# Kernel tuning notes

Measured on AMD Instinct MI355X. Metric: run time of the kernel, lower is better.

The kernel has to match this reference:

```python
import jax, jax.numpy as jnp
import numpy as np

NUM_USER = 100000
NUM_ITEM = 50000
EMBED_DIM = 64
NUM_LAYER = 3
NUM_INTERACTIONS = 1600000  # symmetrized -> nnz = 3.2M
BATCH = 4096


def setup_inputs() -> dict:
    key = jax.random.key(0)
    k1, k2, k3, k4, k5, k6 = jax.random.split(key, 6)
    N = NUM_USER + NUM_ITEM
    user_emb = jax.random.normal(k1, (NUM_USER, EMBED_DIM), dtype=jnp.float32) / EMBED_DIM
    item_emb = jax.random.normal(k2, (NUM_ITEM, EMBED_DIM), dtype=jnp.float32) / EMBED_DIM
    # random bipartite interactions, symmetrized adjacency
    u = jax.random.randint(k3, (NUM_INTERACTIONS,), 0, NUM_USER, dtype=jnp.int32)
    i = jax.random.randint(k4, (NUM_INTERACTIONS,), 0, NUM_ITEM, dtype=jnp.int32) + NUM_USER
    adj_rows = jnp.concatenate([u, i])  # [nnz]
    adj_cols = jnp.concatenate([i, u])  # [nnz]
    # symmetric normalization D^-1/2 A D^-1/2
    deg = jax.ops.segment_sum(jnp.ones_like(adj_rows, dtype=jnp.float32), adj_rows, num_segments=N)
    deg = jnp.maximum(deg, 1.0)
    inv_sqrt = 1.0 / jnp.sqrt(deg)
    adj_vals = inv_sqrt[adj_rows] * inv_sqrt[adj_cols]
    user_ids = jax.random.randint(k5, (BATCH,), 0, NUM_USER, dtype=jnp.int32)
    item_ids = jax.random.randint(k6, (BATCH,), 0, NUM_ITEM, dtype=jnp.int32)
    return {"user_emb": user_emb, "item_emb": item_emb, "adj_vals": adj_vals,
            "adj_rows": adj_rows, "adj_cols": adj_cols,
            "user_ids": user_ids, "item_ids": item_ids}


def reference(user_emb, item_emb, adj_vals, adj_rows, adj_cols, user_ids, item_ids):
    num_user = user_emb.shape[0]
    N = num_user + item_emb.shape[0]
    x = jnp.concatenate([user_emb, item_emb], axis=0)  # [N, D]
    acc = x  # running sum == stack+mean over layers, fused
    for _ in range(NUM_LAYER):
        # SpMM: out[r] += vals * x[c]
        x = jax.ops.segment_sum(adj_vals[:, None] * x[adj_cols], adj_rows, num_segments=N)
        acc = acc + x
    emb = acc / (NUM_LAYER + 1)
    batch_user = emb[user_ids]                  # [B, D]
    batch_item = emb[num_user + item_ids]       # [B, D]
    scores = jnp.sum(batch_user * batch_item, axis=-1)  # DotProdScorer
    return scores
```

## Files before the change

kernel.cpp:

```cpp
#include <hip/hip_runtime.h>


#define DIM 64
#define TSHIFT 8
#define TMASK ((1 << TSHIFT) - 1)
#define TPAD 768
#define EWG 6272
#define STAGE_CAP 6272
#define NREP 4
#define RSTR 2560
#define TSTRIDE 10240
#define NI4 7

typedef unsigned short u16;
typedef unsigned char u8;
typedef unsigned int u32;
typedef unsigned int uv4 __attribute__((ext_vector_type(4)));
typedef float f2 __attribute__((ext_vector_type(2)));

__device__ __forceinline__ u32 f2bf(float f) {
  u32 u = __float_as_uint(f);
  return (u + 0x7FFFu + ((u >> 16) & 1u)) >> 16;
}
__device__ __forceinline__ float bflo(u32 u) {
  return __uint_as_float(u << 16);
}
__device__ __forceinline__ float bfhi(u32 u) {
  return __uint_as_float(u & 0xFFFF0000u);
}
__device__ __forceinline__ f2 up2(u32 u) {
  f2 r;
  r.x = bflo(u);
  r.y = bfhi(u);
  return r;
}

__device__ __forceinline__ int block_incl_scan(int lsum, int tid, int* wsum) {
  int lane = tid & 63, wv = tid >> 6;
  int v = lsum;
#pragma unroll
  for (int off = 1; off < 64; off <<= 1) {
    int t = __shfl_up(v, off, 64);
    if (lane >= off) v += t;
  }
  __syncthreads();
  if (lane == 63) wsum[wv] = v;
  __syncthreads();
  int add = 0;
  if (wv > 0) add += wsum[0];
  if (wv > 1) add += wsum[1];
  if (wv > 2) add += wsum[2];
  return v + add;
}


__global__ __launch_bounds__(256) void partition_direct(
    const int* __restrict__ rows, const int* __restrict__ cols, int nnz,
    int T, int* __restrict__ tcur, u32* __restrict__ bucket) {
  __shared__ u32 sorted[STAGE_CAP];
  __shared__ u16 sortedt[STAGE_CAP];
  __shared__ int cnt[TPAD], lstart[TPAD], gbase[TPAD];
  __shared__ int wsum[4];
  int w = blockIdx.x, tid = threadIdx.x;
  int rep = w & (NREP - 1);
  int j0 = tid * 3;
  cnt[j0] = 0; cnt[j0 + 1] = 0; cnt[j0 + 2] = 0;
  __syncthreads();
  int base = w * EWG;
  int end = min(base + EWG, nnz);
  int total = end - base;
  if (total <= 0) return;
  int nv = total >> 2;
  const int4* r4 = (const int4*)(rows + base);
  const int4* c4 = (const int4*)(cols + base);
  int4 rr[NI4];
#pragma unroll
  for (int j = 0; j < NI4; ++j) {
    int i = tid + j * 256;
    if (i < nv) {
      int4 r = r4[i];
      rr[j] = r;
      atomicAdd(&cnt[r.x >> TSHIFT], 1);
      atomicAdd(&cnt[r.y >> TSHIFT], 1);
      atomicAdd(&cnt[r.z >> TSHIFT], 1);
      atomicAdd(&cnt[r.w >> TSHIFT], 1);
    }
  }
  for (int e = base + (nv << 2) + tid; e < end; e += 256)
    atomicAdd(&cnt[rows[e] >> TSHIFT], 1);
  __syncthreads();
  int c0 = cnt[j0], c1 = cnt[j0 + 1], c2 = cnt[j0 + 2];
  int lsum = c0 + c1 + c2;
  int incl = block_incl_scan(lsum, tid, wsum);
  int excl = incl - lsum;
  lstart[j0] = excl;
  lstart[j0 + 1] = excl + c0;
  lstart[j0 + 2] = excl + c0 + c1;
  if (c0 > 0)
    gbase[j0] = j0 * TSTRIDE + rep * RSTR + atomicAdd(&tcur[j0 * NREP + rep], c0);
  if (c1 > 0)
    gbase[j0 + 1] = (j0 + 1) * TSTRIDE + rep * RSTR +
                    atomicAdd(&tcur[(j0 + 1) * NREP + rep], c1);
  if (c2 > 0)
    gbase[j0 + 2] = (j0 + 2) * TSTRIDE + rep * RSTR +
                    atomicAdd(&tcur[(j0 + 2) * NREP + rep], c2);
  cnt[j0] = 0; cnt[j0 + 1] = 0; cnt[j0 + 2] = 0;
  __syncthreads();
#pragma unroll
  for (int j = 0; j < NI4; ++j) {
    int i = tid + j * 256;
    if (i < nv) {
      int4 r = rr[j];
      int4 c = c4[i];
      int t, s, d;
      t = r.x >> TSHIFT; s = atomicAdd(&cnt[t], 1); d = lstart[t] + s;
      sorted[d] = ((u32)(r.x & TMASK) << 18) | (u32)c.x; sortedt[d] = (u16)t;
      t = r.y >> TSHIFT; s = atomicAdd(&cnt[t], 1); d = lstart[t] + s;
      sorted[d] = ((u32)(r.y & TMASK) << 18) | (u32)c.y; sortedt[d] = (u16)t;
      t = r.z >> TSHIFT; s = atomicAdd(&cnt[t], 1); d = lstart[t] + s;
      sorted[d] = ((u32)(r.z & TMASK) << 18) | (u32)c.z; sortedt[d] = (u16)t;
      t = r.w >> TSHIFT; s = atomicAdd(&cnt[t], 1); d = lstart[t] + s;
      sorted[d] = ((u32)(r.w & TMASK) << 18) | (u32)c.w; sortedt[d] = (u16)t;
    }
  }
  for (int e = base + (nv << 2) + tid; e < end; e += 256) {
    int r = rows[e];
    int c = cols[e];
    int t = r >> TSHIFT;
    int s = atomicAdd(&cnt[t], 1);
    int d = lstart[t] + s;
    sorted[d] = ((u32)(r & TMASK) << 18) | (u32)c;
    sortedt[d] = (u16)t;
  }
  __syncthreads();
  for (int i = tid; i < total; i += 256) {
    int t = sortedt[i];
    bucket[(size_t)gbase[t] + (i - lstart[t])] = sorted[i];
  }
}


__global__ __launch_bounds__(256) void build_csr_y0(
    const u32* __restrict__ bucket, const int* __restrict__ tcur, int T,
    int U, int N, const float4* __restrict__ ue, const float4* __restrict__ ie,
    int* __restrict__ row_ptr, u32* __restrict__ csr,
    uint4* __restrict__ y0b) {
  __shared__ int tl[TPAD];
  __shared__ int hist[256];
  __shared__ int cur[256];
  __shared__ int wsum[4];
  int b = blockIdx.x;
  int t = (b & 1) ? (T - 1 - (b >> 1)) : (b >> 1);
  int tid = threadIdx.x;
  int j0 = tid * 3;
  int v0 = 0, v1 = 0, v2 = 0;
  if (j0 < T) {
    int4 q = ((const int4*)tcur)[j0];
    v0 = q.x + q.y + q.z + q.w;
  }
  if (j0 + 1 < T) {
    int4 q = ((const int4*)tcur)[j0 + 1];
    v1 = q.x + q.y + q.z + q.w;
  }
  if (j0 + 2 < T) {
    int4 q = ((const int4*)tcur)[j0 + 2];
    v2 = q.x + q.y + q.z + q.w;
  }
  int lsum = v0 + v1 + v2;
  int incl0 = block_incl_scan(lsum, tid, wsum);
  int excl0 = incl0 - lsum;
  tl[j0] = excl0 + v0;
  tl[j0 + 1] = excl0 + v0 + v1;
  tl[j0 + 2] = excl0 + v0 + v1 + v2;
  hist[tid] = 0;
  __syncthreads();
  int tbase = (t == 0) ? 0 : tl[t - 1];
  int4 rl = ((const int4*)tcur)[t];
#pragma unroll
  for (int rep = 0; rep < NREP; ++rep) {
    int len = (rep == 0) ? rl.x : (rep == 1) ? rl.y : (rep == 2) ? rl.z : rl.w;
    int rs = t * TSTRIDE + rep * RSTR;
    const uint4* b4 = (const uint4*)(bucket + rs);
    int nv = len >> 2;
    for (int i = tid; i < nv; i += 256) {
      uint4 e = b4[i];
      atomicAdd(&hist[e.x >> 18], 1);
      atomicAdd(&hist[e.y >> 18], 1);
      atomicAdd(&hist[e.z >> 18], 1);
      atomicAdd(&hist[e.w >> 18], 1);
    }
    for (int i = rs + (nv << 2) + tid; i < rs + len; i += 256)
      atomicAdd(&hist[bucket[i] >> 18], 1);
  }
  __syncthreads();
  int h = hist[tid];
  int incl = block_incl_scan(h, tid, wsum);
  int r = (t << TSHIFT) + tid;
  if (r < N) row_ptr[r + 1] = tbase + incl;
  if (t == 0 && tid == 0) row_ptr[0] = 0;
  if (b == 0 && tid < 8)
    y0b[(size_t)N * 8 + tid] = make_uint4(0, 0, 0, 0);
  cur[tid] = tbase + incl - h;
  __syncthreads();
  for (int pass = 0; pass < 8; ++pass) {
    int lr = pass * 32 + (tid >> 3);
    int q = tid & 7;
    int row = (t << TSHIFT) + lr;
    if (row < N) {
      float invs = rsqrtf((float)max(hist[lr], 1));
      const float4* src = (row < U) ? (ue + (size_t)row * 16 + q * 2)
                                    : (ie + (size_t)(row - U) * 16 + q * 2);
      float4 a = src[0], bb = src[1];
      uint4 o;
      o.x = f2bf(a.x * invs) | (f2bf(a.y * invs) << 16);
      o.y = f2bf(a.z * invs) | (f2bf(a.w * invs) << 16);
      o.z = f2bf(bb.x * invs) | (f2bf(bb.y * invs) << 16);
      o.w = f2bf(bb.z * invs) | (f2bf(bb.w * invs) << 16);
      y0b[(size_t)row * 8 + q] = o;
    }
  }
#pragma unroll
  for (int rep = 0; rep < NREP; ++rep) {
    int len = (rep == 0) ? rl.x : (rep == 1) ? rl.y : (rep == 2) ? rl.z : rl.w;
    int rs = t * TSTRIDE + rep * RSTR;
    const uint4* b4 = (const uint4*)(bucket + rs);
    int nv = len >> 2;
    for (int i = tid; i < nv; i += 256) {
      uint4 e = b4[i];
      csr[atomicAdd(&cur[e.x >> 18], 1)] = e.x & 0x3FFFFu;
      csr[atomicAdd(&cur[e.y >> 18], 1)] = e.y & 0x3FFFFu;
      csr[atomicAdd(&cur[e.z >> 18], 1)] = e.z & 0x3FFFFu;
      csr[atomicAdd(&cur[e.w >> 18], 1)] = e.w & 0x3FFFFu;
    }
    for (int i = rs + (nv << 2) + tid; i < rs + len; i += 256) {
      u32 e = bucket[i];
      csr[atomicAdd(&cur[e >> 18], 1)] = e & 0x3FFFFu;
    }
  }
}


__device__ __forceinline__ void load_stage(
    u32 (&c)[8], uv4 (&g)[8], int k, int d, int s,
    const u32* __restrict__ csr, const char* __restrict__ yb, u32 soff,
    int n) {
#pragma unroll
  for (int j = 0; j < 8; ++j) c[j] = (k + j < d) ? csr[s + k + j] : (u32)n;
#pragma unroll
  for (int j = 0; j < 8; ++j)
    g[j] = *(const uv4*)(yb + (size_t)(((size_t)c[j] << 7) | soff));
}

#define ACC_STAGE(G)                                                         \
  _Pragma("unroll") for (int j = 0; j < 8; ++j) {                            \
    a0 += up2(G[j].x);                                                       \
    a1 += up2(G[j].y);                                                       \
    a2 += up2(G[j].z);                                                       \
    a3 += up2(G[j].w);                                                       \
  }

__global__ __launch_bounds__(256, 4) void spmm_sum(
    const int* __restrict__ row_ptr, const u32* __restrict__ csr,
    const u16* __restrict__ yin, u16* __restrict__ yout, int n) {
  if (blockIdx.x == 0 && threadIdx.x < 8)
    ((uint4*)(yout + (size_t)n * DIM))[threadIdx.x] = make_uint4(0, 0, 0, 0);
  int row = (blockIdx.x * 256 + threadIdx.x) >> 3;
  int q8 = threadIdx.x & 7;
  if (row >= n) return;
  int s = row_ptr[row];
  int d = row_ptr[row + 1] - s;
  const char* yb = (const char*)yin;
  u32 soff = (u32)q8 << 4;
  f2 a0 = 0.f, a1 = 0.f, a2 = 0.f, a3 = 0.f;
  u32 cA[8], cB[8];
  uv4 gA[8], gB[8];
  if (d > 0) {
    load_stage(cA, gA, 0, d, s, csr, yb, soff, n);
    int k = 8;
    while (k < d) {
      load_stage(cB, gB, k, d, s, csr, yb, soff, n);
      k += 8;
      ACC_STAGE(gA)
      if (k >= d) {
        ACC_STAGE(gB)
        goto done;
      }
      load_stage(cA, gA, k, d, s, csr, yb, soff, n);
      k += 8;
      ACC_STAGE(gB)
    }
    ACC_STAGE(gA)
  }
done:;
  float inv = 1.0f / (float)max(d, 1);
  uint4 o;
  o.x = f2bf(a0.x * inv) | (f2bf(a0.y * inv) << 16);
  o.y = f2bf(a1.x * inv) | (f2bf(a1.y * inv) << 16);
  o.z = f2bf(a2.x * inv) | (f2bf(a2.y * inv) << 16);
  o.w = f2bf(a3.x * inv) | (f2bf(a3.y * inv) << 16);
  ((uint4*)(yout + (size_t)row * DIM))[q8] = o;
}


#define ACC8(G)                                                              \
  s0 += bflo(G.x); s1 += bfhi(G.x);                                          \
  s2 += bflo(G.y); s3 += bfhi(G.y);                                          \
  s4 += bflo(G.z); s5 += bfhi(G.z);                                          \
  s6 += bflo(G.w); s7 += bfhi(G.w);

__device__ __forceinline__ void gather8(
    const int* __restrict__ row_ptr, const u32* __restrict__ csr,
    const u16* __restrict__ y, int row, int s, int q8, int n, float* o) {
  int start = row_ptr[row];
  int end = row_ptr[row + 1];
  float s0 = 0.f, s1 = 0.f, s2 = 0.f, s3 = 0.f;
  float s4 = 0.f, s5 = 0.f, s6 = 0.f, s7 = 0.f;
  for (int k = start + s; k < end; k += 16) {
    int k2 = k + 8;
    bool ok2 = k2 < end;
    u32 c0 = csr[k];
    u32 c1 = ok2 ? csr[k2] : (u32)n;
    uint4 g0 = ((const uint4*)(y + (size_t)c0 * DIM))[q8];
    uint4 g1 = ((const uint4*)(y + (size_t)c1 * DIM))[q8];
    ACC8(g0) ACC8(g1)
  }
  for (int m = 8; m <= 32; m <<= 1) {
    s0 += __shfl_xor(s0, m, 64); s1 += __shfl_xor(s1, m, 64);
    s2 += __shfl_xor(s2, m, 64); s3 += __shfl_xor(s3, m, 64);
    s4 += __shfl_xor(s4, m, 64); s5 += __shfl_xor(s5, m, 64);
    s6 += __shfl_xor(s6, m, 64); s7 += __shfl_xor(s7, m, 64);
  }
  o[0] = s0; o[1] = s1; o[2] = s2; o[3] = s3;
  o[4] = s4; o[5] = s5; o[6] = s6; o[7] = s7;
}

__global__ __launch_bounds__(256) void spmm3_score(
    const int* __restrict__ row_ptr, const u32* __restrict__ csr,
    const float* __restrict__ ue, const float* __restrict__ ie,
    const u16* __restrict__ y1b, const u16* __restrict__ y2b,
    const int* __restrict__ user_ids, const int* __restrict__ item_ids,
    int U, int N, int batch, float* __restrict__ out) {
  __shared__ float ab[2][2][64];
  int tid = threadIdx.x;
  int pl = tid >> 7;
  int side = (tid >> 6) & 1;
  int lane = tid & 63;
  int w = blockIdx.x * 2 + pl;
  bool active = w < batch;
  int s = lane >> 3;
  int q8 = lane & 7;
  if (active) {
    int u = user_ids[w];
    int iti = item_ids[w];
    int row = (side == 0) ? u : iti + U;
    float g[8];
    gather8(row_ptr, csr, y2b, row, s, q8, N, g);
    int dd = row_ptr[row + 1] - row_ptr[row];
    float sd = sqrtf((float)max(dd, 1)), rd = 1.0f / sd;
    const float4* pe = (side == 0)
                           ? (const float4*)(ue + (size_t)u * DIM) + q8 * 2
                           : (const float4*)(ie + (size_t)iti * DIM) + q8 * 2;
    float4 ea = pe[0], eb = pe[1];
    uint4 y1v = ((const uint4*)(y1b + (size_t)row * DIM))[q8];
    uint4 y2v = ((const uint4*)(y2b + (size_t)row * DIM))[q8];
    if (s == 0) {
      float* dst = &ab[pl][side][q8 * 8];
      dst[0] = ea.x + sd * (bflo(y1v.x) + bflo(y2v.x)) + rd * g[0];
      dst[1] = ea.y + sd * (bfhi(y1v.x) + bfhi(y2v.x)) + rd * g[1];
      dst[2] = ea.z + sd * (bflo(y1v.y) + bflo(y2v.y)) + rd * g[2];
      dst[3] = ea.w + sd * (bfhi(y1v.y) + bfhi(y2v.y)) + rd * g[3];
      dst[4] = eb.x + sd * (bflo(y1v.z) + bflo(y2v.z)) + rd * g[4];
      dst[5] = eb.y + sd * (bfhi(y1v.z) + bfhi(y2v.z)) + rd * g[5];
      dst[6] = eb.z + sd * (bflo(y1v.w) + bflo(y2v.w)) + rd * g[6];
      dst[7] = eb.w + sd * (bfhi(y1v.w) + bfhi(y2v.w)) + rd * g[7];
    }
  }
  __syncthreads();
  if (active && side == 0) {
    float p = ab[pl][0][lane] * ab[pl][1][lane];
    p += __shfl_xor(p, 1, 64);
    p += __shfl_xor(p, 2, 64);
    p += __shfl_xor(p, 4, 64);
    p += __shfl_xor(p, 8, 64);
    p += __shfl_xor(p, 16, 64);
    p += __shfl_xor(p, 32, 64);
    if (lane == 0) out[w] = p * (1.0f / 16.0f);
  }
}

extern "C" void kernel_launch(void* const* d_in, const int* in_sizes, int n_in,
                              void* d_out, int out_size, void* d_ws, size_t ws_size,
                              hipStream_t stream) {
  const float* user_emb = (const float*)d_in[0];
  const float* item_emb = (const float*)d_in[1];
  const int* adj_rows = (const int*)d_in[3];
  const int* adj_cols = (const int*)d_in[4];
  const int* user_ids = (const int*)d_in[5];
  const int* item_ids = (const int*)d_in[6];
  float* scores = (float*)d_out;

  const int U = in_sizes[0] / DIM;
  const int I = in_sizes[1] / DIM;
  const int N = U + I;
  const int nnz = in_sizes[2];
  const int B = in_sizes[5];

  const int T = (N + TMASK) >> TSHIFT;
  const int npw = (nnz + EWG - 1) / EWG;

  char* p = (char*)d_ws;
  auto carve = [&](size_t bytes) {
    void* r = (void*)p;
    p += (bytes + 255) & ~(size_t)255;
    return r;
  };
  u16* y0b = (u16*)carve((size_t)(N + 1) * DIM * 2);
  u16* y1b = (u16*)carve((size_t)(N + 1) * DIM * 2);
  u16* y2b = (u16*)carve((size_t)(N + 1) * DIM * 2);
  int* row_ptr = (int*)carve((size_t)(N + 1) * 4);
  int* tcur = (int*)carve((size_t)T * NREP * 4);
  u32* bucket = (u32*)carve((size_t)(T + 1) * TSTRIDE * 4);
  u32* csr = (u32*)carve((size_t)nnz * 4);

  hipMemsetAsync(tcur, 0, (size_t)T * NREP * 4, stream);

  partition_direct<<<npw, 256, 0, stream>>>(adj_rows, adj_cols, nnz, T, tcur,
                                            bucket);

  build_csr_y0<<<T, 256, 0, stream>>>(bucket, tcur, T, U, N,
                                      (const float4*)user_emb,
                                      (const float4*)item_emb, row_ptr,
                                      csr, (uint4*)y0b);

  const int sblocks = (N * 8 + 255) / 256;
  spmm_sum<<<sblocks, 256, 0, stream>>>(row_ptr, csr, y0b, y1b, N);
  spmm_sum<<<sblocks, 256, 0, stream>>>(row_ptr, csr, y1b, y2b, N);

  spmm3_score<<<(B + 1) / 2, 256, 0, stream>>>(row_ptr, csr, user_emb,
                                               item_emb, y1b, y2b, user_ids,
                                               item_ids, U, N, B, scores);
}
```

Baseline: 265.9 us.

## Fuse all stages into one persistent kernel with software grid barriers

Replaces the five separate kernel launches (partition, CSR build, two SpMM passes, scoring) with a single persistent kernel of fixed grid size that runs each stage in turn, separated by atomic-counter grid barriers. A shared-memory union lets each phase reuse the same LDS. The aim is to remove launch gaps and per-kernel tail drain. In exchange it depends on all 768 blocks being co-resident to avoid deadlock, the larger LDS footprint may lower occupancy in the SpMM phases, and those phases now loop over virtual blocks.

```diff
diff --git a/kernel.cpp b/kernel.cpp
--- a/kernel.cpp
+++ b/kernel.cpp
@@ -11,6 +11,7 @@
 #define RSTR 2560
 #define TSTRIDE 10240
 #define NI4 7
+#define GRID 768
 
 typedef unsigned short u16;
 typedef unsigned char u8;
@@ -33,6 +34,34 @@
   r.x = bflo(u);
   r.y = bfhi(u);
   return r;
+}
+
+union SM {
+  struct {
+    u32 sorted[STAGE_CAP];
+    u16 sortedt[STAGE_CAP];
+    int cnt[TPAD], lstart[TPAD], gbase[TPAD], wsum[4];
+  } part;
+  struct {
+    int tl[TPAD], hist[256], cur[256], wsum[4];
+  } bld;
+  struct {
+    float ab[2][2][64];
+  } sc;
+};
+
+__device__ __forceinline__ void grid_barrier(int* g_arrive, int target) {
+  __syncthreads();
+  if (threadIdx.x == 0) {
+    __threadfence();
+    __hip_atomic_fetch_add(g_arrive, 1, __ATOMIC_ACQ_REL,
+                           __HIP_MEMORY_SCOPE_AGENT);
+    while (__hip_atomic_load(g_arrive, __ATOMIC_ACQUIRE,
+                             __HIP_MEMORY_SCOPE_AGENT) < target)
+      __builtin_amdgcn_s_sleep(8);
+    __threadfence();
+  }
+  __syncthreads();
 }
 
 __device__ __forceinline__ int block_incl_scan(int lsum, int tid, int* wsum) {
@@ -54,192 +83,6 @@
 }
 
 
-__global__ __launch_bounds__(256) void partition_direct(
-    const int* __restrict__ rows, const int* __restrict__ cols, int nnz,
-    int T, int* __restrict__ tcur, u32* __restrict__ bucket) {
-  __shared__ u32 sorted[STAGE_CAP];
-  __shared__ u16 sortedt[STAGE_CAP];
-  __shared__ int cnt[TPAD], lstart[TPAD], gbase[TPAD];
-  __shared__ int wsum[4];
-  int w = blockIdx.x, tid = threadIdx.x;
-  int rep = w & (NREP - 1);
-  int j0 = tid * 3;
-  cnt[j0] = 0; cnt[j0 + 1] = 0; cnt[j0 + 2] = 0;
-  __syncthreads();
-  int base = w * EWG;
-  int end = min(base + EWG, nnz);
-  int total = end - base;
-  if (total <= 0) return;
-  int nv = total >> 2;
-  const int4* r4 = (const int4*)(rows + base);
-  const int4* c4 = (const int4*)(cols + base);
-  int4 rr[NI4];
-#pragma unroll
-  for (int j = 0; j < NI4; ++j) {
-    int i = tid + j * 256;
-    if (i < nv) {
-      int4 r = r4[i];
-      rr[j] = r;
-      atomicAdd(&cnt[r.x >> TSHIFT], 1);
-      atomicAdd(&cnt[r.y >> TSHIFT], 1);
-      atomicAdd(&cnt[r.z >> TSHIFT], 1);
-      atomicAdd(&cnt[r.w >> TSHIFT], 1);
-    }
-  }
-  for (int e = base + (nv << 2) + tid; e < end; e += 256)
-    atomicAdd(&cnt[rows[e] >> TSHIFT], 1);
-  __syncthreads();
-  int c0 = cnt[j0], c1 = cnt[j0 + 1], c2 = cnt[j0 + 2];
-  int lsum = c0 + c1 + c2;
-  int incl = block_incl_scan(lsum, tid, wsum);
-  int excl = incl - lsum;
-  lstart[j0] = excl;
-  lstart[j0 + 1] = excl + c0;
-  lstart[j0 + 2] = excl + c0 + c1;
-  if (c0 > 0)
-    gbase[j0] = j0 * TSTRIDE + rep * RSTR + atomicAdd(&tcur[j0 * NREP + rep], c0);
-  if (c1 > 0)
-    gbase[j0 + 1] = (j0 + 1) * TSTRIDE + rep * RSTR +
-                    atomicAdd(&tcur[(j0 + 1) * NREP + rep], c1);
-  if (c2 > 0)
-    gbase[j0 + 2] = (j0 + 2) * TSTRIDE + rep * RSTR +
-                    atomicAdd(&tcur[(j0 + 2) * NREP + rep], c2);
-  cnt[j0] = 0; cnt[j0 + 1] = 0; cnt[j0 + 2] = 0;
-  __syncthreads();
-#pragma unroll
-  for (int j = 0; j < NI4; ++j) {
-    int i = tid + j * 256;
-    if (i < nv) {
-      int4 r = rr[j];
-      int4 c = c4[i];
-      int t, s, d;
-      t = r.x >> TSHIFT; s = atomicAdd(&cnt[t], 1); d = lstart[t] + s;
-      sorted[d] = ((u32)(r.x & TMASK) << 18) | (u32)c.x; sortedt[d] = (u16)t;
-      t = r.y >> TSHIFT; s = atomicAdd(&cnt[t], 1); d = lstart[t] + s;
-      sorted[d] = ((u32)(r.y & TMASK) << 18) | (u32)c.y; sortedt[d] = (u16)t;
-      t = r.z >> TSHIFT; s = atomicAdd(&cnt[t], 1); d = lstart[t] + s;
-      sorted[d] = ((u32)(r.z & TMASK) << 18) | (u32)c.z; sortedt[d] = (u16)t;
-      t = r.w >> TSHIFT; s = atomicAdd(&cnt[t], 1); d = lstart[t] + s;
-      sorted[d] = ((u32)(r.w & TMASK) << 18) | (u32)c.w; sortedt[d] = (u16)t;
-    }
-  }
-  for (int e = base + (nv << 2) + tid; e < end; e += 256) {
-    int r = rows[e];
-    int c = cols[e];
-    int t = r >> TSHIFT;
-    int s = atomicAdd(&cnt[t], 1);
-    int d = lstart[t] + s;
-    sorted[d] = ((u32)(r & TMASK) << 18) | (u32)c;
-    sortedt[d] = (u16)t;
-  }
-  __syncthreads();
-  for (int i = tid; i < total; i += 256) {
-    int t = sortedt[i];
-    bucket[(size_t)gbase[t] + (i - lstart[t])] = sorted[i];
-  }
-}
-
-
-__global__ __launch_bounds__(256) void build_csr_y0(
-    const u32* __restrict__ bucket, const int* __restrict__ tcur, int T,
-    int U, int N, const float4* __restrict__ ue, const float4* __restrict__ ie,
-    int* __restrict__ row_ptr, u32* __restrict__ csr,
-    uint4* __restrict__ y0b) {
-  __shared__ int tl[TPAD];
-  __shared__ int hist[256];
-  __shared__ int cur[256];
-  __shared__ int wsum[4];
-  int b = blockIdx.x;
-  int t = (b & 1) ? (T - 1 - (b >> 1)) : (b >> 1);
-  int tid = threadIdx.x;
-  int j0 = tid * 3;
-  int v0 = 0, v1 = 0, v2 = 0;
-  if (j0 < T) {
-    int4 q = ((const int4*)tcur)[j0];
-    v0 = q.x + q.y + q.z + q.w;
-  }
-  if (j0 + 1 < T) {
-    int4 q = ((const int4*)tcur)[j0 + 1];
-    v1 = q.x + q.y + q.z + q.w;
-  }
-  if (j0 + 2 < T) {
-    int4 q = ((const int4*)tcur)[j0 + 2];
-    v2 = q.x + q.y + q.z + q.w;
-  }
-  int lsum = v0 + v1 + v2;
-  int incl0 = block_incl_scan(lsum, tid, wsum);
-  int excl0 = incl0 - lsum;
-  tl[j0] = excl0 + v0;
-  tl[j0 + 1] = excl0 + v0 + v1;
-  tl[j0 + 2] = excl0 + v0 + v1 + v2;
-  hist[tid] = 0;
-  __syncthreads();
-  int tbase = (t == 0) ? 0 : tl[t - 1];
-  int4 rl = ((const int4*)tcur)[t];
-#pragma unroll
-  for (int rep = 0; rep < NREP; ++rep) {
-    int len = (rep == 0) ? rl.x : (rep == 1) ? rl.y : (rep == 2) ? rl.z : rl.w;
-    int rs = t * TSTRIDE + rep * RSTR;
-    const uint4* b4 = (const uint4*)(bucket + rs);
-    int nv = len >> 2;
-    for (int i = tid; i < nv; i += 256) {
-      uint4 e = b4[i];
-      atomicAdd(&hist[e.x >> 18], 1);
-      atomicAdd(&hist[e.y >> 18], 1);
-      atomicAdd(&hist[e.z >> 18], 1);
-      atomicAdd(&hist[e.w >> 18], 1);
-    }
-    for (int i = rs + (nv << 2) + tid; i < rs + len; i += 256)
-      atomicAdd(&hist[bucket[i] >> 18], 1);
-  }
-  __syncthreads();
-  int h = hist[tid];
-  int incl = block_incl_scan(h, tid, wsum);
-  int r = (t << TSHIFT) + tid;
-  if (r < N) row_ptr[r + 1] = tbase + incl;
-  if (t == 0 && tid == 0) row_ptr[0] = 0;
-  if (b == 0 && tid < 8)
-    y0b[(size_t)N * 8 + tid] = make_uint4(0, 0, 0, 0);
-  cur[tid] = tbase + incl - h;
-  __syncthreads();
-  for (int pass = 0; pass < 8; ++pass) {
-    int lr = pass * 32 + (tid >> 3);
-    int q = tid & 7;
-    int row = (t << TSHIFT) + lr;
-    if (row < N) {
-      float invs = rsqrtf((float)max(hist[lr], 1));
-      const float4* src = (row < U) ? (ue + (size_t)row * 16 + q * 2)
-                                    : (ie + (size_t)(row - U) * 16 + q * 2);
-      float4 a = src[0], bb = src[1];
-      uint4 o;
-      o.x = f2bf(a.x * invs) | (f2bf(a.y * invs) << 16);
-      o.y = f2bf(a.z * invs) | (f2bf(a.w * invs) << 16);
-      o.z = f2bf(bb.x * invs) | (f2bf(bb.y * invs) << 16);
-      o.w = f2bf(bb.z * invs) | (f2bf(bb.w * invs) << 16);
-      y0b[(size_t)row * 8 + q] = o;
-    }
-  }
-#pragma unroll
-  for (int rep = 0; rep < NREP; ++rep) {
-    int len = (rep == 0) ? rl.x : (rep == 1) ? rl.y : (rep == 2) ? rl.z : rl.w;
-    int rs = t * TSTRIDE + rep * RSTR;
-    const uint4* b4 = (const uint4*)(bucket + rs);
-    int nv = len >> 2;
-    for (int i = tid; i < nv; i += 256) {
-      uint4 e = b4[i];
-      csr[atomicAdd(&cur[e.x >> 18], 1)] = e.x & 0x3FFFFu;
-      csr[atomicAdd(&cur[e.y >> 18], 1)] = e.y & 0x3FFFFu;
-      csr[atomicAdd(&cur[e.z >> 18], 1)] = e.z & 0x3FFFFu;
-      csr[atomicAdd(&cur[e.w >> 18], 1)] = e.w & 0x3FFFFu;
-    }
-    for (int i = rs + (nv << 2) + tid; i < rs + len; i += 256) {
-      u32 e = bucket[i];
-      csr[atomicAdd(&cur[e >> 18], 1)] = e & 0x3FFFFu;
-    }
-  }
-}
-
-
 __device__ __forceinline__ void load_stage(
     u32 (&c)[8], uv4 (&g)[8], int k, int d, int s,
     const u32* __restrict__ csr, const char* __restrict__ yb, u32 soff,
@@ -259,46 +102,49 @@
     a3 += up2(G[j].w);                                                       \
   }
 
-__global__ __launch_bounds__(256, 4) void spmm_sum(
-    const int* __restrict__ row_ptr, const u32* __restrict__ csr,
-    const u16* __restrict__ yin, u16* __restrict__ yout, int n) {
+__device__ void spmm_phase(const int* __restrict__ row_ptr,
+                           const u32* __restrict__ csr,
+                           const u16* __restrict__ yin,
+                           u16* __restrict__ yout, int n, int sblocks) {
   if (blockIdx.x == 0 && threadIdx.x < 8)
     ((uint4*)(yout + (size_t)n * DIM))[threadIdx.x] = make_uint4(0, 0, 0, 0);
-  int row = (blockIdx.x * 256 + threadIdx.x) >> 3;
-  int q8 = threadIdx.x & 7;
-  if (row >= n) return;
-  int s = row_ptr[row];
-  int d = row_ptr[row + 1] - s;
-  const char* yb = (const char*)yin;
-  u32 soff = (u32)q8 << 4;
-  f2 a0 = 0.f, a1 = 0.f, a2 = 0.f, a3 = 0.f;
-  u32 cA[8], cB[8];
-  uv4 gA[8], gB[8];
-  if (d > 0) {
-    load_stage(cA, gA, 0, d, s, csr, yb, soff, n);
-    int k = 8;
-    while (k < d) {
-      load_stage(cB, gB, k, d, s, csr, yb, soff, n);
-      k += 8;
+  for (int vb = blockIdx.x; vb < sblocks; vb += GRID) {
+    int row = (vb * 256 + threadIdx.x) >> 3;
+    int q8 = threadIdx.x & 7;
+    if (row >= n) continue;
+    int s = row_ptr[row];
+    int d = row_ptr[row + 1] - s;
+    const char* yb = (const char*)yin;
+    u32 soff = (u32)q8 << 4;
+    f2 a0 = 0.f, a1 = 0.f, a2 = 0.f, a3 = 0.f;
+    u32 cA[8], cB[8];
+    uv4 gA[8], gB[8];
+    if (d > 0) {
+      load_stage(cA, gA, 0, d, s, csr, yb, soff, n);
+      int k = 8;
+      while (k < d) {
+        load_stage(cB, gB, k, d, s, csr, yb, soff, n);
+        k += 8;
+        ACC_STAGE(gA)
+        if (k >= d) {
+          ACC_STAGE(gB)
+          goto done;
+        }
+        load_stage(cA, gA, k, d, s, csr, yb, soff, n);
+        k += 8;
+        ACC_STAGE(gB)
+      }
       ACC_STAGE(gA)
-      if (k >= d) {
-        ACC_STAGE(gB)
-        goto done;
-      }
-      load_stage(cA, gA, k, d, s, csr, yb, soff, n);
-      k += 8;
-      ACC_STAGE(gB)
     }
-    ACC_STAGE(gA)
-  }
-done:;
-  float inv = 1.0f / (float)max(d, 1);
-  uint4 o;
-  o.x = f2bf(a0.x * inv) | (f2bf(a0.y * inv) << 16);
-  o.y = f2bf(a1.x * inv) | (f2bf(a1.y * inv) << 16);
-  o.z = f2bf(a2.x * inv) | (f2bf(a2.y * inv) << 16);
-  o.w = f2bf(a3.x * inv) | (f2bf(a3.y * inv) << 16);
-  ((uint4*)(yout + (size_t)row * DIM))[q8] = o;
+  done:;
+    float inv = 1.0f / (float)max(d, 1);
+    uint4 o;
+    o.x = f2bf(a0.x * inv) | (f2bf(a0.y * inv) << 16);
+    o.y = f2bf(a1.x * inv) | (f2bf(a1.y * inv) << 16);
+    o.z = f2bf(a2.x * inv) | (f2bf(a2.y * inv) << 16);
+    o.w = f2bf(a3.x * inv) | (f2bf(a3.y * inv) << 16);
+    ((uint4*)(yout + (size_t)row * DIM))[q8] = o;
+  }
 }
 
 
@@ -334,79 +180,279 @@
   o[4] = s4; o[5] = s5; o[6] = s6; o[7] = s7;
 }
 
-__global__ __launch_bounds__(256) void spmm3_score(
-    const int* __restrict__ row_ptr, const u32* __restrict__ csr,
-    const float* __restrict__ ue, const float* __restrict__ ie,
-    const u16* __restrict__ y1b, const u16* __restrict__ y2b,
-    const int* __restrict__ user_ids, const int* __restrict__ item_ids,
-    int U, int N, int batch, float* __restrict__ out) {
-  __shared__ float ab[2][2][64];
+
+__global__ __launch_bounds__(256, 3) void lightgcn_fused(
+    const int* __restrict__ rows, const int* __restrict__ cols, int nnz,
+    int T, int npw, const float4* __restrict__ ue,
+    const float4* __restrict__ ie, const int* __restrict__ user_ids,
+    const int* __restrict__ item_ids, int U, int N, int B,
+    int* __restrict__ tcur, int* g_arrive, u32* __restrict__ bucket,
+    int* __restrict__ row_ptr, u32* __restrict__ csr, u16* __restrict__ y0b,
+    u16* __restrict__ y1b, u16* __restrict__ y2b, float* __restrict__ out) {
+  __shared__ SM sm;
   int tid = threadIdx.x;
-  int pl = tid >> 7;
-  int side = (tid >> 6) & 1;
-  int lane = tid & 63;
-  int w = blockIdx.x * 2 + pl;
-  bool active = w < batch;
-  int s = lane >> 3;
-  int q8 = lane & 7;
-  if (active) {
-    int u = user_ids[w];
-    int iti = item_ids[w];
-    int row = (side == 0) ? u : iti + U;
-    float g[8];
-    gather8(row_ptr, csr, y2b, row, s, q8, N, g);
-    int dd = row_ptr[row + 1] - row_ptr[row];
-    float sd = sqrtf((float)max(dd, 1)), rd = 1.0f / sd;
-    const float4* pe = (side == 0)
-                           ? (const float4*)(ue + (size_t)u * DIM) + q8 * 2
-                           : (const float4*)(ie + (size_t)iti * DIM) + q8 * 2;
-    float4 ea = pe[0], eb = pe[1];
-    uint4 y1v = ((const uint4*)(y1b + (size_t)row * DIM))[q8];
-    uint4 y2v = ((const uint4*)(y2b + (size_t)row * DIM))[q8];
-    if (s == 0) {
-      float* dst = &ab[pl][side][q8 * 8];
-      dst[0] = ea.x + sd * (bflo(y1v.x) + bflo(y2v.x)) + rd * g[0];
-      dst[1] = ea.y + sd * (bfhi(y1v.x) + bfhi(y2v.x)) + rd * g[1];
-      dst[2] = ea.z + sd * (bflo(y1v.y) + bflo(y2v.y)) + rd * g[2];
-      dst[3] = ea.w + sd * (bfhi(y1v.y) + bfhi(y2v.y)) + rd * g[3];
-      dst[4] = eb.x + sd * (bflo(y1v.z) + bflo(y2v.z)) + rd * g[4];
-      dst[5] = eb.y + sd * (bfhi(y1v.z) + bfhi(y2v.z)) + rd * g[5];
-      dst[6] = eb.z + sd * (bflo(y1v.w) + bflo(y2v.w)) + rd * g[6];
-      dst[7] = eb.w + sd * (bfhi(y1v.w) + bfhi(y2v.w)) + rd * g[7];
+
+  {
+    int w = blockIdx.x;
+    if (w < npw) {
+      int rep = w & (NREP - 1);
+      int j0 = tid * 3;
+      sm.part.cnt[j0] = 0; sm.part.cnt[j0 + 1] = 0; sm.part.cnt[j0 + 2] = 0;
+      __syncthreads();
+      int base = w * EWG;
+      int end = min(base + EWG, nnz);
+      int total = end - base;
+      int nv = total >> 2;
+      const int4* r4 = (const int4*)(rows + base);
+      const int4* c4 = (const int4*)(cols + base);
+      int4 rr[NI4];
+#pragma unroll
+      for (int j = 0; j < NI4; ++j) {
+        int i = tid + j * 256;
+        if (i < nv) {
+          int4 r = r4[i];
+          rr[j] = r;
+          atomicAdd(&sm.part.cnt[r.x >> TSHIFT], 1);
+          atomicAdd(&sm.part.cnt[r.y >> TSHIFT], 1);
+          atomicAdd(&sm.part.cnt[r.z >> TSHIFT], 1);
+          atomicAdd(&sm.part.cnt[r.w >> TSHIFT], 1);
+        }
+      }
+      for (int e = base + (nv << 2) + tid; e < end; e += 256)
+        atomicAdd(&sm.part.cnt[rows[e] >> TSHIFT], 1);
+      __syncthreads();
+      int c0 = sm.part.cnt[j0], c1 = sm.part.cnt[j0 + 1],
+          c2 = sm.part.cnt[j0 + 2];
+      int lsum = c0 + c1 + c2;
+      int incl = block_incl_scan(lsum, tid, sm.part.wsum);
+      int excl = incl - lsum;
+      sm.part.lstart[j0] = excl;
+      sm.part.lstart[j0 + 1] = excl + c0;
+      sm.part.lstart[j0 + 2] = excl + c0 + c1;
+      if (c0 > 0)
+        sm.part.gbase[j0] = j0 * TSTRIDE + rep * RSTR +
+                            atomicAdd(&tcur[j0 * NREP + rep], c0);
+      if (c1 > 0)
+        sm.part.gbase[j0 + 1] = (j0 + 1) * TSTRIDE + rep * RSTR +
+                                atomicAdd(&tcur[(j0 + 1) * NREP + rep], c1);
+      if (c2 > 0)
+        sm.part.gbase[j0 + 2] = (j0 + 2) * TSTRIDE + rep * RSTR +
+                                atomicAdd(&tcur[(j0 + 2) * NREP + rep], c2);
+      sm.part.cnt[j0] = 0; sm.part.cnt[j0 + 1] = 0; sm.part.cnt[j0 + 2] = 0;
+      __syncthreads();
+#pragma unroll
+      for (int j = 0; j < NI4; ++j) {
+        int i = tid + j * 256;
+        if (i < nv) {
+          int4 r = rr[j];
+          int4 c = c4[i];
+          int t, s, d;
+          t = r.x >> TSHIFT; s = atomicAdd(&sm.part.cnt[t], 1);
+          d = sm.part.lstart[t] + s;
+          sm.part.sorted[d] = ((u32)(r.x & TMASK) << 18) | (u32)c.x;
+          sm.part.sortedt[d] = (u16)t;
+          t = r.y >> TSHIFT; s = atomicAdd(&sm.part.cnt[t], 1);
+          d = sm.part.lstart[t] + s;
+          sm.part.sorted[d] = ((u32)(r.y & TMASK) << 18) | (u32)c.y;
+          sm.part.sortedt[d] = (u16)t;
+          t = r.z >> TSHIFT; s = atomicAdd(&sm.part.cnt[t], 1);
+          d = sm.part.lstart[t] + s;
+          sm.part.sorted[d] = ((u32)(r.z & TMASK) << 18) | (u32)c.z;
+          sm.part.sortedt[d] = (u16)t;
+          t = r.w >> TSHIFT; s = atomicAdd(&sm.part.cnt[t], 1);
+          d = sm.part.lstart[t] + s;
+          sm.part.sorted[d] = ((u32)(r.w & TMASK) << 18) | (u32)c.w;
+          sm.part.sortedt[d] = (u16)t;
+        }
+      }
+      for (int e = base + (nv << 2) + tid; e < end; e += 256) {
+        int r = rows[e];
+        int c = cols[e];
+        int t = r >> TSHIFT;
+        int s = atomicAdd(&sm.part.cnt[t], 1);
+        int d = sm.part.lstart[t] + s;
+        sm.part.sorted[d] = ((u32)(r & TMASK) << 18) | (u32)c;
+        sm.part.sortedt[d] = (u16)t;
+      }
+      __syncthreads();
+      for (int i = tid; i < total; i += 256) {
+        int t = sm.part.sortedt[i];
+        bucket[(size_t)sm.part.gbase[t] + (i - sm.part.lstart[t])] =
+            sm.part.sorted[i];
+      }
     }
   }
-  __syncthreads();
-  if (active && side == 0) {
-    float p = ab[pl][0][lane] * ab[pl][1][lane];
-    p += __shfl_xor(p, 1, 64);
-    p += __shfl_xor(p, 2, 64);
-    p += __shfl_xor(p, 4, 64);
-    p += __shfl_xor(p, 8, 64);
-    p += __shfl_xor(p, 16, 64);
-    p += __shfl_xor(p, 32, 64);
-    if (lane == 0) out[w] = p * (1.0f / 16.0f);
+  grid_barrier(g_arrive, GRID);
+
+  {
+    int b = blockIdx.x;
+    if (b < T) {
+      int t = (b & 1) ? (T - 1 - (b >> 1)) : (b >> 1);
+      int j0 = tid * 3;
+      int v0 = 0, v1 = 0, v2 = 0;
+      if (j0 < T) {
+        int4 q = ((const int4*)tcur)[j0];
+        v0 = q.x + q.y + q.z + q.w;
+      }
+      if (j0 + 1 < T) {
+        int4 q = ((const int4*)tcur)[j0 + 1];
+        v1 = q.x + q.y + q.z + q.w;
+      }
+      if (j0 + 2 < T) {
+        int4 q = ((const int4*)tcur)[j0 + 2];
+        v2 = q.x + q.y + q.z + q.w;
+      }
+      int lsum = v0 + v1 + v2;
+      int incl0 = block_incl_scan(lsum, tid, sm.bld.wsum);
+      int excl0 = incl0 - lsum;
+      sm.bld.tl[j0] = excl0 + v0;
+      sm.bld.tl[j0 + 1] = excl0 + v0 + v1;
+      sm.bld.tl[j0 + 2] = excl0 + v0 + v1 + v2;
+      sm.bld.hist[tid] = 0;
+      __syncthreads();
+      int tbase = (t == 0) ? 0 : sm.bld.tl[t - 1];
+      int4 rl = ((const int4*)tcur)[t];
+#pragma unroll
+      for (int rep = 0; rep < NREP; ++rep) {
+        int len =
+            (rep == 0) ? rl.x : (rep == 1) ? rl.y : (rep == 2) ? rl.z : rl.w;
+        int rs = t * TSTRIDE + rep * RSTR;
+        const uint4* b4 = (const uint4*)(bucket + rs);
+        int nv = len >> 2;
+        for (int i = tid; i < nv; i += 256) {
+          uint4 e = b4[i];
+          atomicAdd(&sm.bld.hist[e.x >> 18], 1);
+          atomicAdd(&sm.bld.hist[e.y >> 18], 1);
+          atomicAdd(&sm.bld.hist[e.z >> 18], 1);
+          atomicAdd(&sm.bld.hist[e.w >> 18], 1);
+        }
+        for (int i = rs + (nv << 2) + tid; i < rs + len; i += 256)
+          atomicAdd(&sm.bld.hist[bucket[i] >> 18], 1);
+      }
+      __syncthreads();
+      int h = sm.bld.hist[tid];
+      int incl = block_incl_scan(h, tid, sm.bld.wsum);
+      int r = (t << TSHIFT) + tid;
+      if (r < N) row_ptr[r + 1] = tbase + incl;
+      if (t == 0 && tid == 0) row_ptr[0] = 0;
+      if (b == 0 && tid < 8)
+        ((uint4*)y0b)[(size_t)N * 8 + tid] = make_uint4(0, 0, 0, 0);
+      sm.bld.cur[tid] = tbase + incl - h;
+      __syncthreads();
+      for (int pass = 0; pass < 8; ++pass) {
+        int lr = pass * 32 + (tid >> 3);
+        int q = tid & 7;
+        int row = (t << TSHIFT) + lr;
+        if (row < N) {
+          float invs = rsqrtf((float)max(sm.bld.hist[lr], 1));
+          const float4* src = (row < U)
+                                  ? (ue + (size_t)row * 16 + q * 2)
+                                  : (ie + (size_t)(row - U) * 16 + q * 2);
+          float4 a = src[0], bb = src[1];
+          uint4 o;
+          o.x = f2bf(a.x * invs) | (f2bf(a.y * invs) << 16);
+          o.y = f2bf(a.z * invs) | (f2bf(a.w * invs) << 16);
+          o.z = f2bf(bb.x * invs) | (f2bf(bb.y * invs) << 16);
+          o.w = f2bf(bb.z * invs) | (f2bf(bb.w * invs) << 16);
+          ((uint4*)y0b)[(size_t)row * 8 + q] = o;
+        }
+      }
+#pragma unroll
+      for (int rep = 0; rep < NREP; ++rep) {
+        int len =
+            (rep == 0) ? rl.x : (rep == 1) ? rl.y : (rep == 2) ? rl.z : rl.w;
+        int rs = t * TSTRIDE + rep * RSTR;
+        const uint4* b4 = (const uint4*)(bucket + rs);
+        int nv = len >> 2;
+        for (int i = tid; i < nv; i += 256) {
+          uint4 e = b4[i];
+          csr[atomicAdd(&sm.bld.cur[e.x >> 18], 1)] = e.x & 0x3FFFFu;
+          csr[atomicAdd(&sm.bld.cur[e.y >> 18], 1)] = e.y & 0x3FFFFu;
+          csr[atomicAdd(&sm.bld.cur[e.z >> 18], 1)] = e.z & 0x3FFFFu;
+          csr[atomicAdd(&sm.bld.cur[e.w >> 18], 1)] = e.w & 0x3FFFFu;
+        }
+        for (int i = rs + (nv << 2) + tid; i < rs + len; i += 256) {
+          u32 e = bucket[i];
+          csr[atomicAdd(&sm.bld.cur[e >> 18], 1)] = e & 0x3FFFFu;
+        }
+      }
+    }
+  }
+  grid_barrier(g_arrive, 2 * GRID);
+
+  const int sblocks = (N * 8 + 255) / 256;
+  spmm_phase(row_ptr, csr, y0b, y1b, N, sblocks);
+  grid_barrier(g_arrive, 3 * GRID);
+  spmm_phase(row_ptr, csr, y1b, y2b, N, sblocks);
+  grid_barrier(g_arrive, 4 * GRID);
+
+  {
+    int pairs = (B + 1) / 2;
+    int pl = tid >> 7;
+    int side = (tid >> 6) & 1;
+    int lane = tid & 63;
+    int s = lane >> 3;
+    int q8 = lane & 7;
+    for (int vb = blockIdx.x; vb < pairs; vb += GRID) {
+      int w = vb * 2 + pl;
+      bool active = w < B;
+      if (active) {
+        int u = user_ids[w];
+        int iti = item_ids[w];
+        int row = (side == 0) ? u : iti + U;
+        float g[8];
+        gather8(row_ptr, csr, y2b, row, s, q8, N, g);
+        int dd = row_ptr[row + 1] - row_ptr[row];
+        float sd = sqrtf((float)max(dd, 1)), rd = 1.0f / sd;
+        const float4* pe = (side == 0) ? ue + (size_t)u * 16 + q8 * 2
+                                       : ie + (size_t)iti * 16 + q8 * 2;
+        float4 ea = pe[0], eb = pe[1];
+        uint4 y1v = ((const uint4*)y1b)[(size_t)row * 8 + q8];
+        uint4 y2v = ((const uint4*)y2b)[(size_t)row * 8 + q8];
+        if (s == 0) {
+          float* dst = &sm.sc.ab[pl][side][q8 * 8];
+          dst[0] = ea.x + sd * (bflo(y1v.x) + bflo(y2v.x)) + rd * g[0];
+          dst[1] = ea.y + sd * (bfhi(y1v.x) + bfhi(y2v.x)) + rd * g[1];
+          dst[2] = ea.z + sd * (bflo(y1v.y) + bflo(y2v.y)) + rd * g[2];
+          dst[3] = ea.w + sd * (bfhi(y1v.y) + bfhi(y2v.y)) + rd * g[3];
+          dst[4] = eb.x + sd * (bflo(y1v.z) + bflo(y2v.z)) + rd * g[4];
+          dst[5] = eb.y + sd * (bfhi(y1v.z) + bfhi(y2v.z)) + rd * g[5];
+          dst[6] = eb.z + sd * (bflo(y1v.w) + bflo(y2v.w)) + rd * g[6];
+          dst[7] = eb.w + sd * (bfhi(y1v.w) + bfhi(y2v.w)) + rd * g[7];
+        }
+      }
+      __syncthreads();
+      if (active && side == 0) {
+        float p = sm.sc.ab[pl][0][lane] * sm.sc.ab[pl][1][lane];
+        p += __shfl_xor(p, 1, 64);
+        p += __shfl_xor(p, 2, 64);
+        p += __shfl_xor(p, 4, 64);
+        p += __shfl_xor(p, 8, 64);
+        p += __shfl_xor(p, 16, 64);
+        p += __shfl_xor(p, 32, 64);
+        if (lane == 0) out[w] = p * (1.0f / 16.0f);
+      }
+      __syncthreads();
+    }
   }
 }
 
 extern "C" void kernel_launch(void* const* d_in, const int* in_sizes, int n_in,
                               void* d_out, int out_size, void* d_ws, size_t ws_size,
                               hipStream_t stream) {
-  const float* user_emb = (const float*)d_in[0];
-  const float* item_emb = (const float*)d_in[1];
   const int* adj_rows = (const int*)d_in[3];
   const int* adj_cols = (const int*)d_in[4];
   const int* user_ids = (const int*)d_in[5];
   const int* item_ids = (const int*)d_in[6];
-  float* scores = (float*)d_out;
-
-  const int U = in_sizes[0] / DIM;
-  const int I = in_sizes[1] / DIM;
-  const int N = U + I;
-  const int nnz = in_sizes[2];
-  const int B = in_sizes[5];
-
-  const int T = (N + TMASK) >> TSHIFT;
-  const int npw = (nnz + EWG - 1) / EWG;
+
+  int U = in_sizes[0] / DIM;
+  int I = in_sizes[1] / DIM;
+  int N = U + I;
+  int nnz = in_sizes[2];
+  int B = in_sizes[5];
+
+  int T = (N + TMASK) >> TSHIFT;
+  int npw = (nnz + EWG - 1) / EWG;
 
   char* p = (char*)d_ws;
   auto carve = [&](size_t bytes) {
@@ -418,25 +464,20 @@
   u16* y1b = (u16*)carve((size_t)(N + 1) * DIM * 2);
   u16* y2b = (u16*)carve((size_t)(N + 1) * DIM * 2);
   int* row_ptr = (int*)carve((size_t)(N + 1) * 4);
-  int* tcur = (int*)carve((size_t)T * NREP * 4);
+  int* ctrl = (int*)carve(((size_t)T * NREP + 64) * 4);
   u32* bucket = (u32*)carve((size_t)(T + 1) * TSTRIDE * 4);
   u32* csr = (u32*)carve((size_t)nnz * 4);
 
-  hipMemsetAsync(tcur, 0, (size_t)T * NREP * 4, stream);
-
-  partition_direct<<<npw, 256, 0, stream>>>(adj_rows, adj_cols, nnz, T, tcur,
-                                            bucket);
-
-  build_csr_y0<<<T, 256, 0, stream>>>(bucket, tcur, T, U, N,
-                                      (const float4*)user_emb,
-                                      (const float4*)item_emb, row_ptr,
-                                      csr, (uint4*)y0b);
-
-  const int sblocks = (N * 8 + 255) / 256;
-  spmm_sum<<<sblocks, 256, 0, stream>>>(row_ptr, csr, y0b, y1b, N);
-  spmm_sum<<<sblocks, 256, 0, stream>>>(row_ptr, csr, y1b, y2b, N);
-
-  spmm3_score<<<(B + 1) / 2, 256, 0, stream>>>(row_ptr, csr, user_emb,
-                                               item_emb, y1b, y2b, user_ids,
-                                               item_ids, U, N, B, scores);
-}
+  int* tcur = ctrl;
+  int* g_arrive = ctrl + T * NREP;
+
+  const float4* uef = (const float4*)d_in[0];
+  const float4* ief = (const float4*)d_in[1];
+  float* scores = (float*)d_out;
+
+  hipMemsetAsync(ctrl, 0, ((size_t)T * NREP + 64) * 4, stream);
+
+  lightgcn_fused<<<GRID, 256, 0, stream>>>(
+      adj_rows, adj_cols, nnz, T, npw, uef, ief, user_ids, item_ids, U, N, B,
+      tcur, g_arrive, bucket, row_ptr, csr, y0b, y1b, y2b, scores);
+}
```

After: 996.6 us. 275% more time.
